# Optimization experiments

Hardware: AMD Instinct MI355X
Metric: run time of the kernel (lower is better)

Reference implementation:

```python
import jax, jax.numpy as jnp
import numpy as np

TAU = 0.8
N, D = 4096, 512

def _proj(x, W, b):
    # nn.Linear then ELU (torch Linear: x @ W.T + b)
    return jax.nn.elu(x @ W.T + b)

def setup_inputs() -> dict:
    key = jax.random.key(0)
    k1, k2, k3, k4, k5 = jax.random.split(key, 5)
    v1 = jax.random.normal(k1, (N, D), dtype=jnp.float32)
    v2 = jax.random.normal(k2, (N, D), dtype=jnp.float32)
    pos = jax.random.uniform(k3, (N, N), dtype=jnp.float32)
    neg = jax.random.uniform(k4, (N, N), dtype=jnp.float32)
    W = jax.random.normal(k5, (D, D), dtype=jnp.float32) * (1.414 / np.sqrt(D))
    b = jnp.zeros((D,), dtype=jnp.float32)
    return {"v1_embs": v1, "v2_embs": v2, "pos": pos, "neg": neg, "W_proj": W, "b_proj": b}

def reference(v1_embs, v2_embs, pos, neg, W_proj, b_proj):
    z1 = _proj(v1_embs, W_proj, b_proj)
    z2 = _proj(v2_embs, W_proj, b_proj)
    # cosine-similarity style: dot / (|z1||z2|) / tau, then exp
    n1 = jnp.linalg.norm(z1, axis=-1, keepdims=True)  # [N,1]
    n2 = jnp.linalg.norm(z2, axis=-1, keepdims=True)  # [N,1]
    dots = z1 @ z2.T                                   # [N,N]
    sim = jnp.exp(dots / (n1 * n2.T) / TAU)
    sim_pos = sim * pos
    sim_neg = sim * neg
    ratio = sim_pos.sum() / (sim_pos + sim_neg).sum()
    return -jnp.log(ratio)
```

## Files before the change

kernel.cpp:

```cpp
#include <hip/hip_runtime.h>
#include <hip/hip_bf16.h>
#include <math.h>

#define NROWS 4096
#define DDIM  512
#define INV_TAU 1.25f

typedef __attribute__((ext_vector_type(8))) short short8;
typedef __attribute__((ext_vector_type(4))) float f32x4;

__device__ inline void gload_lds16(const void* g, void* l) {
  __builtin_amdgcn_global_load_lds(
      (const __attribute__((address_space(1))) void*)g,
      (__attribute__((address_space(3))) void*)l, 16, 0, 0);
}

__device__ inline unsigned short f2bf(float f) {
  __hip_bfloat16 h = __float2bfloat16(f);
  return __builtin_bit_cast(unsigned short, h);
}
__device__ inline float bf2f(unsigned short u) {
  return __bfloat162float(__builtin_bit_cast(__hip_bfloat16, u));
}

__global__ void convert_kernel(const float* __restrict__ v1,
                               const float* __restrict__ v2,
                               const float* __restrict__ W,
                               unsigned short* __restrict__ v1b,
                               unsigned short* __restrict__ v2b,
                               unsigned short* __restrict__ Wb,
                               float* __restrict__ nsq1,
                               float* __restrict__ nsq2) {
  int idx = blockIdx.x * blockDim.x + threadIdx.x;
  if (idx < NROWS) { nsq1[idx] = 0.f; nsq2[idx] = 0.f; }
  const int TOTV = (NROWS * DDIM) / 4;
  const int TOTW = (DDIM * DDIM) / 4;
  const int total = 2 * TOTV + TOTW;
  const int stride = gridDim.x * blockDim.x;
  for (int i = idx; i < total; i += stride) {
    const float4* src; unsigned short* dst; int j;
    if (i < TOTV)            { src = (const float4*)v1; dst = v1b; j = i; }
    else if (i < 2 * TOTV)   { src = (const float4*)v2; dst = v2b; j = i - TOTV; }
    else                     { src = (const float4*)W;  dst = Wb;  j = i - 2 * TOTV; }
    float4 x = src[j];
    ushort4 o;
    o.x = f2bf(x.x); o.y = f2bf(x.y); o.z = f2bf(x.z); o.w = f2bf(x.w);
    *(ushort4*)&dst[j * 4] = o;
  }
}

#define MM_CORE(Ag, Bg)                                                        \
  {                                                                            \
    for (int kt = 0; kt < DDIM; kt += 32) {                                    \
      _Pragma("unroll")                                                        \
      for (int i = 0; i < 2; ++i) {                                            \
        int off = i * 4096 + tid * 16;            \
        int row = off >> 6;                       \
        int kb  = off & 63;                                                    \
        gload_lds16((const char*)((Ag) + row * DDIM + kt) + kb,                \
                    (char*)As + i * 4096 + wid * 1024);                        \
        gload_lds16((const char*)((Bg) + row * DDIM + kt) + kb,                \
                    (char*)Bs + i * 4096 + wid * 1024);                        \
      }                                                                        \
      asm volatile("s_waitcnt vmcnt(0)" ::: "memory");                         \
      __syncthreads();                                                         \
      short8 av[4], bv[4];                                                     \
      _Pragma("unroll")                                                        \
      for (int m = 0; m < 4; ++m)                                              \
        av[m] = *(const short8*)&As[(wm * 64 + m * 16 + l15) * 32 + l4 * 8];   \
      _Pragma("unroll")                                                        \
      for (int n = 0; n < 4; ++n)                                              \
        bv[n] = *(const short8*)&Bs[(wn * 64 + n * 16 + l15) * 32 + l4 * 8];   \
      _Pragma("unroll")                                                        \
      for (int m = 0; m < 4; ++m)                                              \
        _Pragma("unroll")                                                      \
        for (int n = 0; n < 4; ++n)                                            \
          acc[m][n] = __builtin_amdgcn_mfma_f32_16x16x32_bf16(                 \
              av[m], bv[n], acc[m][n], 0, 0, 0);                               \
      __syncthreads();                                                         \
    }                                                                          \
  }

__global__ __launch_bounds__(256) void proj_kernel(
    const unsigned short* __restrict__ v1b, const unsigned short* __restrict__ v2b,
    const unsigned short* __restrict__ Wb,  const float* __restrict__ bias,
    unsigned short* __restrict__ z1b, unsigned short* __restrict__ z2b,
    float* __restrict__ nsq1, float* __restrict__ nsq2) {
  __shared__ __align__(16) unsigned short As[128 * 32];
  __shared__ __align__(16) unsigned short Bs[128 * 32];
  const int tid = threadIdx.x;
  const int wid = tid >> 6, lane = tid & 63;
  const int wm = wid >> 1, wn = wid & 1;
  const int l15 = lane & 15, l4 = lane >> 4;

  const int zsel = blockIdx.z;
  const unsigned short* Ag = (zsel ? v2b : v1b) + (size_t)blockIdx.y * 128 * DDIM;
  const unsigned short* Bg = Wb + (size_t)blockIdx.x * 128 * DDIM;
  unsigned short* Z = (zsel ? z2b : z1b);
  float* nsq = (zsel ? nsq2 : nsq1);

  f32x4 acc[4][4];
#pragma unroll
  for (int m = 0; m < 4; ++m)
#pragma unroll
    for (int n = 0; n < 4; ++n) acc[m][n] = (f32x4){0.f, 0.f, 0.f, 0.f};

  MM_CORE(Ag, Bg);

  const int rowBase = blockIdx.y * 128 + wm * 64;
  const int colBase = blockIdx.x * 128 + wn * 64;
  float bcol[4];
#pragma unroll
  for (int n = 0; n < 4; ++n) bcol[n] = bias[colBase + n * 16 + l15];
#pragma unroll
  for (int m = 0; m < 4; ++m) {
#pragma unroll
    for (int reg = 0; reg < 4; ++reg) {
      int gRow = rowBase + m * 16 + l4 * 4 + reg;
      float rs = 0.f;
#pragma unroll
      for (int n = 0; n < 4; ++n) {
        int gCol = colBase + n * 16 + l15;
        float y = acc[m][n][reg] + bcol[n];
        float zv = (y > 0.f) ? y : expm1f(y);
        unsigned short zb = f2bf(zv);
        Z[(size_t)gRow * DDIM + gCol] = zb;
        float zf = bf2f(zb);
        rs += zf * zf;
      }
      rs += __shfl_xor(rs, 1, 64);
      rs += __shfl_xor(rs, 2, 64);
      rs += __shfl_xor(rs, 4, 64);
      rs += __shfl_xor(rs, 8, 64);
      if (l15 == 0) atomicAdd(&nsq[gRow], rs);
    }
  }
}

__global__ __launch_bounds__(256) void dots_kernel(
    const unsigned short* __restrict__ z1b, const unsigned short* __restrict__ z2b,
    const float* __restrict__ nsq1, const float* __restrict__ nsq2,
    const float* __restrict__ pos, const float* __restrict__ neg,
    double* __restrict__ partials) {
  __shared__ __align__(16) unsigned short As[128 * 32];
  __shared__ __align__(16) unsigned short Bs[128 * 32];
  const int tid = threadIdx.x;
  const int wid = tid >> 6, lane = tid & 63;
  const int wm = wid >> 1, wn = wid & 1;
  const int l15 = lane & 15, l4 = lane >> 4;

  const unsigned short* Ag = z1b + (size_t)blockIdx.y * 128 * DDIM;
  const unsigned short* Bg = z2b + (size_t)blockIdx.x * 128 * DDIM;

  f32x4 acc[4][4];
#pragma unroll
  for (int m = 0; m < 4; ++m)
#pragma unroll
    for (int n = 0; n < 4; ++n) acc[m][n] = (f32x4){0.f, 0.f, 0.f, 0.f};

  MM_CORE(Ag, Bg);

  const int rowBase = blockIdx.y * 128 + wm * 64;
  const int colBase = blockIdx.x * 128 + wn * 64;
  float n2s[4];
  int gCol[4];
#pragma unroll
  for (int n = 0; n < 4; ++n) {
    gCol[n] = colBase + n * 16 + l15;
    n2s[n] = nsq2[gCol[n]];
  }
  float sumP = 0.f, sumT = 0.f;
#pragma unroll
  for (int m = 0; m < 4; ++m) {
#pragma unroll
    for (int reg = 0; reg < 4; ++reg) {
      int gRow = rowBase + m * 16 + l4 * 4 + reg;
      float r1 = nsq1[gRow];
      const float* prow = pos + (size_t)gRow * NROWS;
      const float* grow = neg + (size_t)gRow * NROWS;
#pragma unroll
      for (int n = 0; n < 4; ++n) {
        float rinv = rsqrtf(r1 * n2s[n]);
        float s = __expf(acc[m][n][reg] * rinv * INV_TAU);
        float p = prow[gCol[n]];
        float g = grow[gCol[n]];
        sumP += s * p;
        sumT += s * (p + g);
      }
    }
  }
#pragma unroll
  for (int sft = 1; sft < 64; sft <<= 1) {
    sumP += __shfl_xor(sumP, sft, 64);
    sumT += __shfl_xor(sumT, sft, 64);
  }
  __shared__ float redP[4], redT[4];
  if (lane == 0) { redP[wid] = sumP; redT[wid] = sumT; }
  __syncthreads();
  if (tid == 0) {
    double tp = (double)redP[0] + redP[1] + redP[2] + redP[3];
    double tt = (double)redT[0] + redT[1] + redT[2] + redT[3];
    int bid = blockIdx.y * gridDim.x + blockIdx.x;
    partials[2 * bid]     = tp;
    partials[2 * bid + 1] = tt;
  }
}

__global__ void finalize_kernel(const double* __restrict__ partials,
                                float* __restrict__ out) {
  __shared__ double sp[256], st[256];
  int t = threadIdx.x;
  double a = 0.0, b = 0.0;
  for (int i = t; i < 1024; i += 256) {
    a += partials[2 * i];
    b += partials[2 * i + 1];
  }
  sp[t] = a; st[t] = b;
  __syncthreads();
  for (int s = 128; s > 0; s >>= 1) {
    if (t < s) { sp[t] += sp[t + s]; st[t] += st[t + s]; }
    __syncthreads();
  }
  if (t == 0) out[0] = (float)(log(st[0]) - log(sp[0]));
}

extern "C" void kernel_launch(void* const* d_in, const int* in_sizes, int n_in,
                              void* d_out, int out_size, void* d_ws, size_t ws_size,
                              hipStream_t stream) {
  (void)in_sizes; (void)n_in; (void)out_size; (void)ws_size;
  const float* v1   = (const float*)d_in[0];
  const float* v2   = (const float*)d_in[1];
  const float* pos  = (const float*)d_in[2];
  const float* neg  = (const float*)d_in[3];
  const float* W    = (const float*)d_in[4];
  const float* bias = (const float*)d_in[5];

  char* ws = (char*)d_ws;
  unsigned short* z1b = (unsigned short*)(ws + 0);
  unsigned short* z2b = (unsigned short*)(ws + 4194304);
  unsigned short* v1b = (unsigned short*)(ws + 8388608);
  unsigned short* v2b = (unsigned short*)(ws + 12582912);
  unsigned short* Wb  = (unsigned short*)(ws + 16777216);
  float* nsq1         = (float*)(ws + 17301504);
  float* nsq2         = (float*)(ws + 17317888);
  double* partials    = (double*)(ws + 17334272);
  float* out = (float*)d_out;

  hipLaunchKernelGGL(convert_kernel, dim3(1024), dim3(256), 0, stream,
                     v1, v2, W, v1b, v2b, Wb, nsq1, nsq2);
  hipLaunchKernelGGL(proj_kernel, dim3(DDIM / 128, NROWS / 128, 2), dim3(256), 0, stream,
                     v1b, v2b, Wb, bias, z1b, z2b, nsq1, nsq2);
  hipLaunchKernelGGL(dots_kernel, dim3(NROWS / 128, NROWS / 128), dim3(256), 0, stream,
                     z1b, z2b, nsq1, nsq2, pos, neg, partials);
  hipLaunchKernelGGL(finalize_kernel, dim3(1), dim3(256), 0, stream,
                     partials, out);
}
```

Measured before the change: 77.96 us.

## Stage sim tile through LDS to coalesce pos/neg reads with float4 loads

The epilogue now writes the exp'd similarity values for each 32-row chunk into shared memory (reusing the GEMM staging buffers with a padded stride), then re-reads them in a row-major thread mapping. That lets each thread load pos/neg with contiguous float4 accesses instead of scattered scalar loads following the MFMA output layout. It also computes reciprocal norms once per row and column rather than an rsqrt per element. The cost is extra LDS traffic and two barriers per chunk, and the shared buffer is aliased with the GEMM operand storage.

Result: no change. 78.86 us (+1.2%).

```diff
diff --git a/kernel.cpp b/kernel.cpp
--- a/kernel.cpp
+++ b/kernel.cpp
@@ -5,6 +5,7 @@
 #define NROWS 4096
 #define DDIM  512
 #define INV_TAU 1.25f
+#define SROW 132
 
 typedef __attribute__((ext_vector_type(8))) short short8;
 typedef __attribute__((ext_vector_type(4))) float f32x4;
@@ -142,8 +143,11 @@
     const float* __restrict__ nsq1, const float* __restrict__ nsq2,
     const float* __restrict__ pos, const float* __restrict__ neg,
     double* __restrict__ partials) {
-  __shared__ __align__(16) unsigned short As[128 * 32];
-  __shared__ __align__(16) unsigned short Bs[128 * 32];
+  __shared__ __align__(16) char smem[32 * SROW * 4];
+  unsigned short* As = (unsigned short*)smem;
+  unsigned short* Bs = (unsigned short*)(smem + 8192);
+  float* sCh = (float*)smem;
+
   const int tid = threadIdx.x;
   const int wid = tid >> 6, lane = tid & 63;
   const int wm = wid >> 1, wn = wid & 1;
@@ -160,35 +164,52 @@
 
   MM_CORE(Ag, Bg);
 
-  const int rowBase = blockIdx.y * 128 + wm * 64;
-  const int colBase = blockIdx.x * 128 + wn * 64;
-  float n2s[4];
-  int gCol[4];
-#pragma unroll
-  for (int n = 0; n < 4; ++n) {
-    gCol[n] = colBase + n * 16 + l15;
-    n2s[n] = nsq2[gCol[n]];
-  }
+  const int blockRow = blockIdx.y * 128;
+  const int blockCol = blockIdx.x * 128;
+  const int rowBase = blockRow + wm * 64;
+  const int colBase = blockCol + wn * 64;
+
+  float rs2[4];
+#pragma unroll
+  for (int n = 0; n < 4; ++n) rs2[n] = rsqrtf(nsq2[colBase + n * 16 + l15]);
+
+  const int lr = tid >> 3;
+  const int lcBase = (tid & 7) * 16;
+  const int gRowRbase = blockRow + (lr >> 4) * 64 + (lr & 15);
+  const int lrW = wm * 16 + l4 * 4;
+  const int lcW = wn * 64 + l15;
+
   float sumP = 0.f, sumT = 0.f;
 #pragma unroll
   for (int m = 0; m < 4; ++m) {
+    const float* pr = pos + (size_t)(gRowRbase + m * 16) * NROWS + blockCol + lcBase;
+    const float* gr = neg + (size_t)(gRowRbase + m * 16) * NROWS + blockCol + lcBase;
+    float4 pv[4], gv[4];
+#pragma unroll
+    for (int i = 0; i < 4; ++i) {
+      pv[i] = *(const float4*)(pr + 4 * i);
+      gv[i] = *(const float4*)(gr + 4 * i);
+    }
 #pragma unroll
     for (int reg = 0; reg < 4; ++reg) {
-      int gRow = rowBase + m * 16 + l4 * 4 + reg;
-      float r1 = nsq1[gRow];
-      const float* prow = pos + (size_t)gRow * NROWS;
-      const float* grow = neg + (size_t)gRow * NROWS;
+      float rs1 = rsqrtf(nsq1[rowBase + m * 16 + l4 * 4 + reg]);
 #pragma unroll
       for (int n = 0; n < 4; ++n) {
-        float rinv = rsqrtf(r1 * n2s[n]);
-        float s = __expf(acc[m][n][reg] * rinv * INV_TAU);
-        float p = prow[gCol[n]];
-        float g = grow[gCol[n]];
-        sumP += s * p;
-        sumT += s * (p + g);
+        float s = __expf(acc[m][n][reg] * (rs1 * rs2[n]) * INV_TAU);
+        sCh[(lrW + reg) * SROW + lcW + n * 16] = s;
       }
     }
-  }
+    __syncthreads();
+#pragma unroll
+    for (int i = 0; i < 4; ++i) {
+      float4 s4 = *(const float4*)&sCh[lr * SROW + lcBase + 4 * i];
+      sumP += s4.x * pv[i].x + s4.y * pv[i].y + s4.z * pv[i].z + s4.w * pv[i].w;
+      sumT += s4.x * (pv[i].x + gv[i].x) + s4.y * (pv[i].y + gv[i].y) +
+              s4.z * (pv[i].z + gv[i].z) + s4.w * (pv[i].w + gv[i].w);
+    }
+    __syncthreads();
+  }
+
 #pragma unroll
   for (int sft = 1; sft < 64; sft <<= 1) {
     sumP += __shfl_xor(sumP, sft, 64);
```
